# Performance work log

Hardware: AMD Instinct MI355X
Metric: run time of the kernel (lower is better)

Reference implementation:

```python
import jax, jax.numpy as jnp
import numpy as np

B, P, E = 256, 196, 2048           # batch, num_pixels, encoder_size
H, A, EMB = 2048, 512, 300         # hidden, attention, embedding dims
V_IN, V_OUT = 262, 261             # input vocab (classes+2), output (classes+1)
T = 7                              # max_seq_len + 2


def setup_inputs() -> dict:
    key = jax.random.key(0)
    ks = jax.random.split(key, 20)
    s = 0.02
    return {
        "encoder_feature_out": jax.random.normal(ks[0], (B, P, E), jnp.float32),
        "encoder_out": jax.random.normal(ks[1], (B, E), jnp.float32),
        "annotations_X": jax.random.randint(ks[2], (B, T), 0, V_IN),
        "is_train": 1,
        "emb_W": jax.random.normal(ks[3], (V_IN, EMB), jnp.float32) * s,
        "feat_W": jax.random.normal(ks[4], (H, E), jnp.float32) * s,
        "feat_b": jnp.zeros((H,), jnp.float32),
        "W_ih": jax.random.normal(ks[5], (4 * H, EMB + E), jnp.float32) * s,
        "W_hh": jax.random.normal(ks[6], (4 * H, H), jnp.float32) * s,
        "b_ih": jnp.zeros((4 * H,), jnp.float32),
        "b_hh": jnp.zeros((4 * H,), jnp.float32),
        "enc_att_W": jax.random.normal(ks[7], (A, E), jnp.float32) * s,
        "enc_att_b": jnp.zeros((A,), jnp.float32),
        "dec_att_W": jax.random.normal(ks[8], (A, H), jnp.float32) * s,
        "dec_att_b": jnp.zeros((A,), jnp.float32),
        "full_att_W": jax.random.normal(ks[9], (1, A), jnp.float32) * s,
        "full_att_b": jnp.zeros((1,), jnp.float32),
        "fbeta_W": jax.random.normal(ks[10], (E, H), jnp.float32) * s,
        "fbeta_b": jnp.zeros((E,), jnp.float32),
        "fc_W": jax.random.normal(ks[11], (V_OUT, H), jnp.float32) * s,
        "fc_b": jnp.zeros((V_OUT,), jnp.float32),
    }


def _forward(encoder_feature_out, encoder_out, annotations_X,
             emb_W, feat_W, feat_b, W_ih, W_hh, b_ih, b_hh,
             enc_att_W, enc_att_b, dec_att_W, dec_att_b,
             full_att_W, full_att_b, fbeta_W, fbeta_b, fc_W, fc_b):
    enc = encoder_feature_out                                  # (B,P,E)
    # encoder side of additive attention is constant across steps
    att1 = jnp.einsum('bpe,ae->bpa', enc, enc_att_W) + enc_att_b  # (B,P,A)
    h0 = encoder_out @ feat_W.T + feat_b                       # (B,H)
    c0 = jnp.zeros_like(h0)

    def step(carry, ann_t):
        h, c = carry
        # additive attention
        att2 = h @ dec_att_W.T + dec_att_b                     # (B,A)
        e = jax.nn.relu(att1 + att2[:, None, :]) @ full_att_W[0] + full_att_b[0]  # (B,P)
        alpha = jax.nn.softmax(e, axis=1)                      # (B,P)
        awe = jnp.einsum('bp,bpe->be', alpha, enc)             # (B,E)
        gate = jax.nn.sigmoid(h @ fbeta_W.T + fbeta_b)         # (B,E)
        awe = gate * awe
        # LSTMCell (dropout layers in eval mode -> identity)
        x = jnp.concatenate([emb_W[ann_t], awe], axis=1)       # (B,EMB+E)
        gates = x @ W_ih.T + b_ih + h @ W_hh.T + b_hh          # (B,4H)
        i, f, g, o = jnp.split(gates, 4, axis=1)
        c = jax.nn.sigmoid(f) * c + jax.nn.sigmoid(i) * jnp.tanh(g)
        h = jax.nn.sigmoid(o) * jnp.tanh(c)
        yhat = h @ fc_W.T + fc_b                               # (B,V_OUT)
        return (h, c), (yhat, alpha)

    _, (yhats, alphas) = jax.lax.scan(step, (h0, c0), annotations_X.T)  # (T,B,...)
    return jnp.transpose(yhats, (1, 0, 2)), jnp.transpose(alphas, (1, 0, 2))


def reference(encoder_feature_out, encoder_out, annotations_X, is_train,
              emb_W, feat_W, feat_b, W_ih, W_hh, b_ih, b_hh,
              enc_att_W, enc_att_b, dec_att_W, dec_att_b,
              full_att_W, full_att_b, fbeta_W, fbeta_b, fc_W, fc_b):
    # is_train=True (teacher forcing) path
    return _forward(encoder_feature_out, encoder_out, annotations_X,
                    emb_W, feat_W, feat_b, W_ih, W_hh, b_ih, b_hh,
                    enc_att_W, enc_att_b, dec_att_W, dec_att_b,
                    full_att_W, full_att_b, fbeta_W, fbeta_b, fc_W, fc_b)
```

## Files before the change

### kernel.cpp

```cpp
#include <hip/hip_runtime.h>
#include <math.h>

#define B_    256
#define P_    196
#define E_    2048
#define H_    2048
#define A_    512
#define EMB_  300
#define VOUT_ 261
#define T_    7

#define KPAD_   4608
#define EMBOFF_ 2048
#define AWEOFF_ 2352

#define NSTEP_  2880
#define FCOFF_  2560
#define GSPLIT_ 4
#define PSPLIT_ 2

typedef __attribute__((ext_vector_type(8))) short          short8_t;
typedef __attribute__((ext_vector_type(8))) unsigned short ushort8_t;
typedef __attribute__((ext_vector_type(4))) float          f32x4;

__device__ __forceinline__ unsigned short f2b(float f) {
    union { float f; unsigned int u; } v; v.f = f;
    unsigned int x = v.u;
    unsigned int r = (x + 0x7fffu + ((x >> 16) & 1u)) >> 16;
    return (unsigned short)r;
}
__device__ __forceinline__ float b2f(unsigned short u) {
    union { unsigned int u; float f; } v; v.u = ((unsigned int)u) << 16;
    return v.f;
}
__device__ __forceinline__ ushort8_t pack8(float4 u0, float4 u1) {
    ushort8_t u;
    u[0]=f2b(u0.x); u[1]=f2b(u0.y); u[2]=f2b(u0.z); u[3]=f2b(u0.w);
    u[4]=f2b(u1.x); u[5]=f2b(u1.y); u[6]=f2b(u1.z); u[7]=f2b(u1.w);
    return u;
}

template<bool SPLITK, bool OUT16, bool XCDSWZ>
__global__ __launch_bounds__(256)
void gemm_sk(const unsigned short* __restrict__ Ab, int lda,
             const unsigned short* __restrict__ Bw, int ldb,
             void* __restrict__ Cout, int ldc,
             int Kper, int colbase, const float* __restrict__ bias, int nbx)
{
    __shared__ ushort8_t As8[256 * 8];
    __shared__ ushort8_t Bs8[64 * 8];

    const int tid  = threadIdx.x;
    const int lane = tid & 63;
    const int w    = tid >> 6;

    int nblk, mblk;
    if (XCDSWZ) {
        const int bid  = blockIdx.x;
        const int pair = (bid & 7) * (gridDim.x >> 3) + (bid >> 3);
        nblk = pair % nbx;
        mblk = pair / nbx;
    } else {
        nblk = blockIdx.x;
        mblk = 0;
    }
    const int col0  = colbase + nblk * 64;
    const int kbase = SPLITK ? blockIdx.y * Kper : 0;
    const int mrow0 = XCDSWZ ? mblk * 256 : 0;

    const int rb  = tid >> 3;
    const int seg = tid & 7;
    const int swz = seg ^ (rb & 7);

    const unsigned short* Ap = Ab + (size_t)(mrow0 + rb) * lda + kbase + seg * 8;
    const unsigned short* Bp = Bw + (size_t)(col0 + rb) * ldb + kbase + seg * 8;

    const int lr = lane & 15;
    const int hi = lane >> 4;

    f32x4 acc[4][4];
    #pragma unroll
    for (int m = 0; m < 4; ++m)
        #pragma unroll
        for (int n = 0; n < 4; ++n)
            acc[m][n] = (f32x4){0.f, 0.f, 0.f, 0.f};

    ushort8_t aR[8], bR[2];
    #pragma unroll
    for (int i = 0; i < 8; ++i)
        aR[i] = *(const ushort8_t*)(Ap + (size_t)i * 32 * lda);
    bR[0] = *(const ushort8_t*)(Bp);
    bR[1] = *(const ushort8_t*)(Bp + (size_t)32 * ldb);

    for (int k0 = 0; k0 < Kper; k0 += 64) {
        __syncthreads();
        #pragma unroll
        for (int i = 0; i < 8; ++i)
            As8[(rb + i * 32) * 8 + swz] = aR[i];
        Bs8[rb * 8 + swz]        = bR[0];
        Bs8[(rb + 32) * 8 + swz] = bR[1];
        __syncthreads();
        if (k0 + 64 < Kper) {
            #pragma unroll
            for (int i = 0; i < 8; ++i)
                aR[i] = *(const ushort8_t*)(Ap + (size_t)i * 32 * lda + k0 + 64);
            bR[0] = *(const ushort8_t*)(Bp + k0 + 64);
            bR[1] = *(const ushort8_t*)(Bp + (size_t)32 * ldb + k0 + 64);
        }
        #pragma unroll
        for (int kc = 0; kc < 2; ++kc) {
            short8_t af[4], bf[4];
            #pragma unroll
            for (int m = 0; m < 4; ++m) {
                const int row = w * 64 + m * 16 + lr;
                af[m] = *(const short8_t*)&As8[row * 8 + ((kc * 4 + hi) ^ (row & 7))];
            }
            #pragma unroll
            for (int n = 0; n < 4; ++n) {
                const int row = n * 16 + lr;
                bf[n] = *(const short8_t*)&Bs8[row * 8 + ((kc * 4 + hi) ^ (row & 7))];
            }
            #pragma unroll
            for (int m = 0; m < 4; ++m)
                #pragma unroll
                for (int n = 0; n < 4; ++n)
                    acc[m][n] = __builtin_amdgcn_mfma_f32_16x16x32_bf16(
                        af[m], bf[n], acc[m][n], 0, 0, 0);
        }
    }

    if (OUT16) {
        unsigned short* C16 = (unsigned short*)Cout;
        #pragma unroll
        for (int m = 0; m < 4; ++m) {
            const int grow0 = mrow0 + w * 64 + m * 16 + hi * 4;
            #pragma unroll
            for (int n = 0; n < 4; ++n) {
                const int gcol = col0 + n * 16 + lr;
                const float bv = bias[gcol];
                #pragma unroll
                for (int r = 0; r < 4; ++r)
                    C16[(size_t)(grow0 + r) * ldc + gcol] = f2b(acc[m][n][r] + bv);
            }
        }
    } else {
        float* Cs = (float*)Cout + (SPLITK ? (size_t)blockIdx.y * 256 * ldc : 0);
        #pragma unroll
        for (int m = 0; m < 4; ++m) {
            const int grow0 = w * 64 + m * 16 + hi * 4;
            #pragma unroll
            for (int n = 0; n < 4; ++n) {
                const int gcol = col0 + n * 16 + lr;
                #pragma unroll
                for (int r = 0; r < 4; ++r)
                    Cs[(size_t)(grow0 + r) * ldc + gcol] = acc[m][n][r];
            }
        }
    }
}

__global__ __launch_bounds__(256)
void gemm_mfma_f32(const float* __restrict__ Af, int lda,
                   const unsigned short* __restrict__ Bw, int ldb,
                   unsigned short* __restrict__ Cp, int ldc,
                   const float* __restrict__ bias,
                   int M, int N, int K)
{
    __shared__ __align__(16) unsigned short As[64][40];
    __shared__ __align__(16) unsigned short Bs[128][40];

    const int tid  = threadIdx.x;
    const int lane = tid & 63;
    const int wid  = tid >> 6;
    const int wr   = wid >> 1;
    const int wc   = wid & 1;
    const int row0 = blockIdx.y * 64;
    const int col0 = blockIdx.x * 128;

    const int ar = tid >> 2;
    const int as = (tid & 3) * 8;
    const int br = tid >> 1;
    const int bs = (tid & 1) * 16;

    const int lr = lane & 15;
    const int lk = (lane >> 4) * 8;

    f32x4 acc[2][4];
    #pragma unroll
    for (int m = 0; m < 2; ++m)
        #pragma unroll
        for (int n = 0; n < 4; ++n)
            acc[m][n] = (f32x4){0.f, 0.f, 0.f, 0.f};

    for (int k0 = 0; k0 < K; k0 += 32) {
        ushort8_t aval = {0,0,0,0,0,0,0,0};
        if (row0 + ar < M) {
            const float* p = Af + (size_t)(row0 + ar) * lda + k0 + as;
            aval = pack8(*(const float4*)(p), *(const float4*)(p + 4));
        }
        ushort8_t bv0 = {0,0,0,0,0,0,0,0}, bv1 = {0,0,0,0,0,0,0,0};
        if (col0 + br < N) {
            const unsigned short* p = Bw + (size_t)(col0 + br) * ldb + k0 + bs;
            bv0 = *(const ushort8_t*)(p);
            bv1 = *(const ushort8_t*)(p + 8);
        }
        __syncthreads();
        *(ushort8_t*)&As[ar][as]     = aval;
        *(ushort8_t*)&Bs[br][bs]     = bv0;
        *(ushort8_t*)&Bs[br][bs + 8] = bv1;
        __syncthreads();

        short8_t af[2], bf[4];
        #pragma unroll
        for (int m = 0; m < 2; ++m)
            af[m] = *(const short8_t*)&As[wr * 32 + m * 16 + lr][lk];
        #pragma unroll
        for (int n = 0; n < 4; ++n)
            bf[n] = *(const short8_t*)&Bs[wc * 64 + n * 16 + lr][lk];
        #pragma unroll
        for (int m = 0; m < 2; ++m)
            #pragma unroll
            for (int n = 0; n < 4; ++n)
                acc[m][n] = __builtin_amdgcn_mfma_f32_16x16x32_bf16(
                    af[m], bf[n], acc[m][n], 0, 0, 0);
    }

    #pragma unroll
    for (int m = 0; m < 2; ++m) {
        const int grow0 = row0 + wr * 32 + m * 16 + (lane >> 4) * 4;
        #pragma unroll
        for (int n = 0; n < 4; ++n) {
            const int gcol = col0 + wc * 64 + n * 16 + lr;
            if (gcol >= N) continue;
            const float bv = bias[gcol];
            #pragma unroll
            for (int r = 0; r < 4; ++r) {
                const int grow = grow0 + r;
                if (grow >= M) continue;
                Cp[(size_t)grow * ldc + gcol] = f2b(acc[m][n][r] + bv);
            }
        }
    }
}

__global__ __launch_bounds__(256)
void cvt_bf16_kernel(const float* __restrict__ in, unsigned short* __restrict__ out,
                     int n8)
{
    const int idx = blockIdx.x * 256 + threadIdx.x;
    if (idx >= n8) return;
    const size_t base = (size_t)idx * 8;
    *(ushort8_t*)(out + base) =
        pack8(*(const float4*)(in + base), *(const float4*)(in + base + 4));
}

__global__ __launch_bounds__(256)
void setup_kernel(const float* __restrict__ b_ih, const float* __restrict__ b_hh,
                  float* __restrict__ bias4h,
                  const float* __restrict__ enc_attW, unsigned short* __restrict__ encattW16,
                  const float* __restrict__ feat_W, unsigned short* __restrict__ featW16,
                  const float* __restrict__ enc_out, unsigned short* __restrict__ encout16,
                  const float* __restrict__ dec_attW, const float* __restrict__ fbeta_W,
                  const float* __restrict__ fc_W, unsigned short* __restrict__ wstep,
                  unsigned short* __restrict__ xcat, float* __restrict__ cbuf)
{
    int bid = blockIdx.x;
    const int tid = threadIdx.x;
    if (bid < 32) {
        const int i = bid * 256 + tid;
        bias4h[i] = b_ih[i] + b_hh[i];
        return;
    }
    bid -= 32;
    if (bid < 512) {
        const size_t base = ((size_t)bid * 256 + tid) * 8;
        *(ushort8_t*)(encattW16 + base) =
            pack8(*(const float4*)(enc_attW + base), *(const float4*)(enc_attW + base + 4));
        return;
    }
    bid -= 512;
    if (bid < 2048) {
        const size_t base = ((size_t)bid * 256 + tid) * 8;
        *(ushort8_t*)(featW16 + base) =
            pack8(*(const float4*)(feat_W + base), *(const float4*)(feat_W + base + 4));
        return;
    }
    bid -= 2048;
    if (bid < 256) {
        const size_t base = ((size_t)bid * 256 + tid) * 8;
        *(ushort8_t*)(encout16 + base) =
            pack8(*(const float4*)(enc_out + base), *(const float4*)(enc_out + base + 4));
        return;
    }
    bid -= 256;
    if (bid < NSTEP_) {
        const int row = bid;
        const int c0  = tid * 8;
        const float* src;
        if (row < A_)                   src = dec_attW + (size_t)row * H_ + c0;
        else if (row < A_ + E_)         src = fbeta_W + (size_t)(row - A_) * H_ + c0;
        else if (row < A_ + E_ + VOUT_) src = fc_W + (size_t)(row - A_ - E_) * H_ + c0;
        else                            src = nullptr;
        ushort8_t u = {0,0,0,0,0,0,0,0};
        if (src) u = pack8(*(const float4*)(src), *(const float4*)(src + 4));
        *(ushort8_t*)(wstep + (size_t)row * H_ + c0) = u;
        return;
    }
    bid -= NSTEP_;
    if (bid < 576) {
        const size_t base = ((size_t)bid * 256 + tid) * 8;
        ushort8_t z = {0,0,0,0,0,0,0,0};
        *(ushort8_t*)(xcat + base) = z;
        return;
    }
    bid -= 576;
    {
        const size_t base = ((size_t)bid * 256 + tid) * 4;
        *(float4*)(cbuf + base) = make_float4(0.f, 0.f, 0.f, 0.f);
    }
}

__global__ __launch_bounds__(256)
void build_wcat_kernel(const float* __restrict__ W_ih, const float* __restrict__ W_hh,
                       unsigned short* __restrict__ wcat)
{
    const int row = blockIdx.x;
    const int LIH = EMB_ + E_;
    for (int s = threadIdx.x; s < KPAD_ / 8; s += 256) {
        const int k0 = s * 8;
        ushort8_t u;
        const float* src = nullptr;
        if (k0 + 8 <= H_)                         src = W_hh + (size_t)row * H_ + k0;
        else if (k0 >= H_ && k0 + 8 <= 2344)      src = W_ih + (size_t)row * LIH + (k0 - H_);
        else if (k0 >= AWEOFF_ && k0 + 8 <= 4400) src = W_ih + (size_t)row * LIH + (k0 - 2052);
        if (src) {
            u = pack8(*(const float4*)(src), *(const float4*)(src + 4));
        } else {
            #pragma unroll
            for (int i = 0; i < 8; ++i) {
                const int k = k0 + i;
                float v = 0.f;
                if (k >= H_ && k < 2348)           v = W_ih[(size_t)row * LIH + (k - H_)];
                else if (k >= AWEOFF_ && k < 4400) v = W_ih[(size_t)row * LIH + (k - 2052)];
                u[i] = f2b(v);
            }
        }
        *(ushort8_t*)(wcat + (size_t)row * KPAD_ + k0) = u;
    }
}

__global__ __launch_bounds__(256)
void reduce_h0(const float* __restrict__ parts, const float* __restrict__ bias,
               unsigned short* __restrict__ xcat)
{
    const int i = blockIdx.x * 256 + threadIdx.x;
    const int row = i >> 11, col = i & (H_ - 1);
    float acc = bias[col];
    #pragma unroll
    for (int s = 0; s < 8; ++s)
        acc += parts[(size_t)s * 256 * H_ + i];
    xcat[(size_t)row * KPAD_ + col] = f2b(acc);
}

__global__ __launch_bounds__(256)
void att_awe_kernel(const float* __restrict__ parts, const float* __restrict__ dec_attb,
                    const unsigned short* __restrict__ att1,
                    const float* __restrict__ fw_g, const float* __restrict__ fb,
                    const float* __restrict__ encf, const unsigned short* __restrict__ enc16,
                    int use16,
                    float* __restrict__ awe_part, float* __restrict__ out_a, int t)
{
    const int ph = blockIdx.x;
    const int b  = blockIdx.y;
    const int tid = threadIdx.x;
    const int lane = tid & 63;
    const int wid  = tid >> 6;
    __shared__ float att2s[A_];
    __shared__ float es[P_];
    __shared__ float red[4];

    #pragma unroll
    for (int it = 0; it < A_ / 256; ++it) {
        const int c = tid + it * 256;
        float acc = dec_attb[c];
        #pragma unroll
        for (int s = 0; s < 8; ++s)
            acc += parts[((size_t)s * B_ + b) * NSTEP_ + c];
        att2s[c] = acc;
    }
    __syncthreads();

    const int l32  = lane & 31;
    const int slot = wid * 2 + (lane >> 5);
    float a2r[16], fwr[16];
    #pragma unroll
    for (int k = 0; k < 16; ++k) {
        a2r[k] = att2s[l32 * 16 + k];
        fwr[k] = fw_g[l32 * 16 + k];
    }
    const float fbv = fb[0];

    for (int p = slot; p < P_; p += 8) {
        const unsigned short* row = att1 + ((size_t)b * P_ + p) * A_ + l32 * 16;
        ushort8_t v0 = *(const ushort8_t*)(row);
        ushort8_t v1 = *(const ushort8_t*)(row + 8);
        float acc = 0.f;
        #pragma unroll
        for (int k = 0; k < 8; ++k) {
            float x = b2f(v0[k]) + a2r[k];
            x = x > 0.f ? x : 0.f;
            acc = fmaf(x, fwr[k], acc);
        }
        #pragma unroll
        for (int k = 0; k < 8; ++k) {
            float x = b2f(v1[k]) + a2r[k + 8];
            x = x > 0.f ? x : 0.f;
            acc = fmaf(x, fwr[k + 8], acc);
        }
        #pragma unroll
        for (int off = 16; off > 0; off >>= 1)
            acc += __shfl_xor(acc, off);
        if (l32 == 0) es[p] = acc + fbv;
    }
    __syncthreads();

    float v = (tid < P_) ? es[tid] : -1e30f;
    float m = v;
    #pragma unroll
    for (int off = 32; off > 0; off >>= 1)
        m = fmaxf(m, __shfl_xor(m, off));
    if (lane == 0) red[wid] = m;
    __syncthreads();
    m = fmaxf(fmaxf(red[0], red[1]), fmaxf(red[2], red[3]));
    __syncthreads();
    float p = (tid < P_) ? expf(v - m) : 0.f;
    float s = p;
    #pragma unroll
    for (int off = 32; off > 0; off >>= 1)
        s += __shfl_xor(s, off);
    if (lane == 0) red[wid] = s;
    __syncthreads();
    s = red[0] + red[1] + red[2] + red[3];
    float alv = p / s;
    if (tid < P_) {
        if (ph == 0)
            out_a[((size_t)b * T_ + t) * P_ + tid] = alv;
    }
    __syncthreads();
    if (tid < P_) es[tid] = alv;
    __syncthreads();

    const int e0 = tid * 8;
    const int prow0 = ph * 98;
    float acc[8] = {0.f,0.f,0.f,0.f,0.f,0.f,0.f,0.f};
    if (use16) {
        const unsigned short* ep = enc16 + ((size_t)b * P_ + prow0) * E_ + e0;
        int pp = 0;
        for (; pp + 4 <= 98; pp += 4) {
            ushort8_t v0 = *(const ushort8_t*)(ep + (size_t)(pp + 0) * E_);
            ushort8_t v1 = *(const ushort8_t*)(ep + (size_t)(pp + 1) * E_);
            ushort8_t v2 = *(const ushort8_t*)(ep + (size_t)(pp + 2) * E_);
            ushort8_t v3 = *(const ushort8_t*)(ep + (size_t)(pp + 3) * E_);
            const float a0 = es[prow0 + pp],     a1 = es[prow0 + pp + 1];
            const float a2 = es[prow0 + pp + 2], a3 = es[prow0 + pp + 3];
            #pragma unroll
            for (int k = 0; k < 8; ++k) {
                float t0 = fmaf(a0, b2f(v0[k]), acc[k]);
                float t1 = fmaf(a1, b2f(v1[k]), t0);
                float t2 = fmaf(a2, b2f(v2[k]), t1);
                acc[k]   = fmaf(a3, b2f(v3[k]), t2);
            }
        }
        for (; pp < 98; ++pp) {
            ushort8_t v0 = *(const ushort8_t*)(ep + (size_t)pp * E_);
            const float a0 = es[prow0 + pp];
            #pragma unroll
            for (int k = 0; k < 8; ++k)
                acc[k] = fmaf(a0, b2f(v0[k]), acc[k]);
        }
    } else {
        const float* ep = encf + ((size_t)b * P_ + prow0) * E_ + e0;
        for (int pp = 0; pp < 98; ++pp) {
            float4 v0 = *(const float4*)(ep + (size_t)pp * E_);
            float4 v1 = *(const float4*)(ep + (size_t)pp * E_ + 4);
            const float a0 = es[prow0 + pp];
            acc[0] = fmaf(a0, v0.x, acc[0]); acc[1] = fmaf(a0, v0.y, acc[1]);
            acc[2] = fmaf(a0, v0.z, acc[2]); acc[3] = fmaf(a0, v0.w, acc[3]);
            acc[4] = fmaf(a0, v1.x, acc[4]); acc[5] = fmaf(a0, v1.y, acc[5]);
            acc[6] = fmaf(a0, v1.z, acc[6]); acc[7] = fmaf(a0, v1.w, acc[7]);
        }
    }
    float* dst = awe_part + ((size_t)ph * B_ + b) * E_ + e0;
    *(float4*)(dst)     = make_float4(acc[0], acc[1], acc[2], acc[3]);
    *(float4*)(dst + 4) = make_float4(acc[4], acc[5], acc[6], acc[7]);
}

__global__ __launch_bounds__(256)
void awe_fin_kernel(const float* __restrict__ parts, const float* __restrict__ fbeta_b,
                    const float* __restrict__ awe_part,
                    const int* __restrict__ ann, const float* __restrict__ embW,
                    unsigned short* __restrict__ xcat,
                    const float* __restrict__ fc_b, float* __restrict__ out_y, int t)
{
    const int b = blockIdx.x;
    const int tid = threadIdx.x;
    const int e0 = tid * 8;

    float aw[8] = {0.f,0.f,0.f,0.f,0.f,0.f,0.f,0.f};
    #pragma unroll
    for (int ph = 0; ph < PSPLIT_; ++ph) {
        float4 pa = *(const float4*)(awe_part + ((size_t)ph * B_ + b) * E_ + e0);
        float4 pb = *(const float4*)(awe_part + ((size_t)ph * B_ + b) * E_ + e0 + 4);
        aw[0] += pa.x; aw[1] += pa.y; aw[2] += pa.z; aw[3] += pa.w;
        aw[4] += pb.x; aw[5] += pb.y; aw[6] += pb.z; aw[7] += pb.w;
    }

    ushort8_t o;
    #pragma unroll
    for (int k = 0; k < 8; ++k) {
        float g = fbeta_b[e0 + k];
        #pragma unroll
        for (int s = 0; s < 8; ++s)
            g += parts[((size_t)s * B_ + b) * NSTEP_ + A_ + e0 + k];
        const float sg = 1.f / (1.f + expf(-g));
        o[k] = f2b(sg * aw[k]);
    }
    *(ushort8_t*)(xcat + (size_t)b * KPAD_ + AWEOFF_ + e0) = o;

    const int r = ann[b * T_ + t];
    for (int j = tid; j < EMB_; j += 256)
        xcat[(size_t)b * KPAD_ + EMBOFF_ + j] = f2b(embW[(size_t)r * EMB_ + j]);

    if (t > 0) {
        for (int c = tid; c < VOUT_; c += 256) {
            float a = fc_b[c];
            #pragma unroll
            for (int s = 0; s < 8; ++s)
                a += parts[((size_t)s * B_ + b) * NSTEP_ + FCOFF_ + c];
            out_y[((size_t)b * T_ + (t - 1)) * VOUT_ + c] = a;
        }
    }
}

__global__ __launch_bounds__(256)
void fc_reduce(const float* __restrict__ parts, const float* __restrict__ fc_b,
               float* __restrict__ out_y, int tm1)
{
    const int i = blockIdx.x * 256 + threadIdx.x;
    if (i >= B_ * VOUT_) return;
    const int b = i / VOUT_;
    const int c = i - b * VOUT_;
    float acc = fc_b[c];
    #pragma unroll
    for (int s = 0; s < 8; ++s)
        acc += parts[((size_t)s * B_ + b) * NSTEP_ + FCOFF_ + c];
    out_y[((size_t)b * T_ + tm1) * VOUT_ + c] = acc;
}

__global__ __launch_bounds__(256)
void lstm_kernel(const float* __restrict__ parts, const float* __restrict__ bias4h,
                 float* __restrict__ c, unsigned short* __restrict__ xcat)
{
    const int idx = blockIdx.x * 256 + threadIdx.x;
    const int b = idx >> 11;
    const int j = idx & (H_ - 1);
    const float* p0 = parts + (size_t)b * 4 * H_;
    const size_t S = (size_t)256 * 4 * H_;
    float gi = bias4h[j],          gf = bias4h[H_ + j];
    float gg = bias4h[2 * H_ + j], go = bias4h[3 * H_ + j];
    #pragma unroll
    for (int s = 0; s < GSPLIT_; ++s) {
        const float* p = p0 + s * S;
        gi += p[j]; gf += p[H_ + j]; gg += p[2 * H_ + j]; go += p[3 * H_ + j];
    }
    const float si = 1.f / (1.f + expf(-gi));
    const float sf = 1.f / (1.f + expf(-gf));
    const float so = 1.f / (1.f + expf(-go));
    const float cn = sf * c[idx] + si * tanhf(gg);
    c[idx] = cn;
    xcat[(size_t)b * KPAD_ + j] = f2b(so * tanhf(cn));
}

extern "C" void kernel_launch(void* const* d_in, const int* in_sizes, int n_in,
                              void* d_out, int out_size, void* d_ws, size_t ws_size,
                              hipStream_t stream)
{
    const float* enc      = (const float*)d_in[0];
    const float* enc_out  = (const float*)d_in[1];
    const int*   ann      = (const int*)  d_in[2];
    const float* emb_W    = (const float*)d_in[4];
    const float* feat_W   = (const float*)d_in[5];
    const float* feat_b   = (const float*)d_in[6];
    const float* W_ih     = (const float*)d_in[7];
    const float* W_hh     = (const float*)d_in[8];
    const float* b_ih     = (const float*)d_in[9];
    const float* b_hh     = (const float*)d_in[10];
    const float* enc_attW = (const float*)d_in[11];
    const float* enc_attb = (const float*)d_in[12];
    const float* dec_attW = (const float*)d_in[13];
    const float* dec_attb = (const float*)d_in[14];
    const float* full_attW= (const float*)d_in[15];
    const float* full_attb= (const float*)d_in[16];
    const float* fbeta_W  = (const float*)d_in[17];
    const float* fbeta_b  = (const float*)d_in[18];
    const float* fc_W     = (const float*)d_in[19];
    const float* fc_b     = (const float*)d_in[20];
    (void)in_sizes; (void)n_in; (void)out_size;

    float* out   = (float*)d_out;
    float* out_y = out;
    float* out_a = out + (size_t)B_ * T_ * VOUT_;

    char* base = (char*)d_ws;
    size_t off = 0;
    auto alloc = [&](size_t bytes) -> char* {
        char* p = base + off;
        off += (bytes + 255) & ~(size_t)255;
        return p;
    };
    unsigned short* att1_16   = (unsigned short*)alloc((size_t)B_ * P_ * A_ * 2);
    unsigned short* wcat16    = (unsigned short*)alloc((size_t)4 * H_ * KPAD_ * 2);
    unsigned short* wstep16   = (unsigned short*)alloc((size_t)NSTEP_ * H_ * 2);
    unsigned short* encattW16 = (unsigned short*)alloc((size_t)A_ * E_ * 2);
    unsigned short* featW16   = (unsigned short*)alloc((size_t)H_ * E_ * 2);
    unsigned short* encout16  = (unsigned short*)alloc((size_t)B_ * E_ * 2);
    unsigned short* xcat16    = (unsigned short*)alloc((size_t)B_ * KPAD_ * 2);
    float* cbuf     = (float*)alloc((size_t)B_ * H_ * 4);
    float* bias4h   = (float*)alloc((size_t)4 * H_ * 4);
    float* awe_part = (float*)alloc((size_t)PSPLIT_ * B_ * E_ * 4);
    const size_t parts_elems = (size_t)GSPLIT_ * B_ * 4 * H_;
    float* parts   = (float*)alloc(parts_elems * 4);
    const size_t enc_elems = (size_t)B_ * P_ * E_;
    const int use16 = (off + enc_elems * 2 <= ws_size) ? 1 : 0;
    unsigned short* enc16 = use16 ? (unsigned short*)alloc(enc_elems * 2) : nullptr;

    const dim3 blk(256);

    setup_kernel<<<dim3(32 + 512 + 2048 + 256 + NSTEP_ + 576 + 512), blk, 0, stream>>>(
        b_ih, b_hh, bias4h, enc_attW, encattW16, feat_W, featW16,
        enc_out, encout16, dec_attW, fbeta_W, fc_W, wstep16, xcat16, cbuf);
    build_wcat_kernel<<<dim3(4 * H_), blk, 0, stream>>>(W_ih, W_hh, wcat16);
    if (use16)
        cvt_bf16_kernel<<<dim3((int)(enc_elems / 8 + 255) / 256), blk, 0, stream>>>(
            enc, enc16, (int)(enc_elems / 8));

    if (use16) {
        gemm_sk<false, true, true><<<dim3(196 * 8), blk, 0, stream>>>(
            enc16, E_, encattW16, E_, att1_16, A_, E_, 0, enc_attb, 8);
    } else {
        dim3 g((A_ + 127) / 128, (B_ * P_) / 64);
        gemm_mfma_f32<<<g, blk, 0, stream>>>(enc, E_, encattW16, E_,
            att1_16, A_, enc_attb, B_ * P_, A_, E_);
    }
    gemm_sk<true, false, false><<<dim3(H_ / 64, 8), blk, 0, stream>>>(
        encout16, E_, featW16, E_, parts, H_, E_ / 8, 0, nullptr, 0);
    reduce_h0<<<dim3(B_ * H_ / 256), blk, 0, stream>>>(parts, feat_b, xcat16);

    for (int t = 0; t <= T_; ++t) {
        if (t < T_)
            gemm_sk<true, false, false><<<dim3(NSTEP_ / 64, 8), blk, 0, stream>>>(
                xcat16, KPAD_, wstep16, H_, parts, NSTEP_, H_ / 8, 0, nullptr, 0);
        else
            gemm_sk<true, false, false><<<dim3((NSTEP_ - FCOFF_) / 64, 8), blk, 0, stream>>>(
                xcat16, KPAD_, wstep16, H_, parts, NSTEP_, H_ / 8, FCOFF_, nullptr, 0);
        if (t == T_) {
            fc_reduce<<<dim3((B_ * VOUT_ + 255) / 256), blk, 0, stream>>>(parts, fc_b, out_y, t - 1);
            break;
        }

        att_awe_kernel<<<dim3(PSPLIT_, B_), blk, 0, stream>>>(
            parts, dec_attb, att1_16, full_attW, full_attb,
            enc, enc16, use16, awe_part, out_a, t);
        awe_fin_kernel<<<dim3(B_), blk, 0, stream>>>(parts, fbeta_b, awe_part,
                                                     ann, emb_W, xcat16, fc_b, out_y, t);

        gemm_sk<true, false, false><<<dim3(4 * H_ / 64, GSPLIT_), blk, 0, stream>>>(
            xcat16, KPAD_, wcat16, KPAD_, parts, 4 * H_, KPAD_ / GSPLIT_, 0, nullptr, 0);
        lstm_kernel<<<dim3(B_ * H_ / 256), blk, 0, stream>>>(parts, bias4h, cbuf, xcat16);
    }
}
```

Baseline: 1.197 ms.

## Double-buffer GEMM tiles with direct global-to-LDS async loads

The bf16 MFMA GEMM now loads its A and B tiles straight from global memory into shared memory with `global_load_lds`, instead of staging them through registers. It ping-pongs two LDS buffers so the next K-slice is fetched while the current one is computed. The XOR swizzle moves from the LDS store address to the global source column, so the LDS read pattern is unchanged. This removes register pressure and the VGPR-to-LDS store instructions, at the cost of double the LDS footprint. The loop assumes an even number of K steps and relies on the barriers correctly waiting for the async loads.

```diff
diff --git a/kernel.cpp b/kernel.cpp
--- a/kernel.cpp
+++ b/kernel.cpp
@@ -40,6 +40,13 @@
     return u;
 }
 
+__device__ __forceinline__ void gld_lds16(const unsigned short* g, const ushort8_t* l) {
+    __builtin_amdgcn_global_load_lds(
+        (const __attribute__((address_space(1))) void*)g,
+        (__attribute__((address_space(3))) void*)l,
+        16, 0, 0);
+}
+
 template<bool SPLITK, bool OUT16, bool XCDSWZ>
 __global__ __launch_bounds__(256)
 void gemm_sk(const unsigned short* __restrict__ Ab, int lda,
@@ -47,8 +54,8 @@
              void* __restrict__ Cout, int ldc,
              int Kper, int colbase, const float* __restrict__ bias, int nbx)
 {
-    __shared__ ushort8_t As8[256 * 8];
-    __shared__ ushort8_t Bs8[64 * 8];
+    __shared__ ushort8_t As8[2][256 * 8];
+    __shared__ ushort8_t Bs8[2][64 * 8];
 
     const int tid  = threadIdx.x;
     const int lane = tid & 63;
@@ -72,8 +79,8 @@
     const int seg = tid & 7;
     const int swz = seg ^ (rb & 7);
 
-    const unsigned short* Ap = Ab + (size_t)(mrow0 + rb) * lda + kbase + seg * 8;
-    const unsigned short* Bp = Bw + (size_t)(col0 + rb) * ldb + kbase + seg * 8;
+    const unsigned short* Ap = Ab + (size_t)(mrow0 + rb) * lda + kbase + swz * 8;
+    const unsigned short* Bp = Bw + (size_t)(col0 + rb) * ldb + kbase + swz * 8;
 
     const int lr = lane & 15;
     const int hi = lane >> 4;
@@ -85,40 +92,29 @@
         for (int n = 0; n < 4; ++n)
             acc[m][n] = (f32x4){0.f, 0.f, 0.f, 0.f};
 
-    ushort8_t aR[8], bR[2];
-    #pragma unroll
-    for (int i = 0; i < 8; ++i)
-        aR[i] = *(const ushort8_t*)(Ap + (size_t)i * 32 * lda);
-    bR[0] = *(const ushort8_t*)(Bp);
-    bR[1] = *(const ushort8_t*)(Bp + (size_t)32 * ldb);
-
-    for (int k0 = 0; k0 < Kper; k0 += 64) {
-        __syncthreads();
+    auto STAGE = [&](int buf, int koff) {
         #pragma unroll
         for (int i = 0; i < 8; ++i)
-            As8[(rb + i * 32) * 8 + swz] = aR[i];
-        Bs8[rb * 8 + swz]        = bR[0];
-        Bs8[(rb + 32) * 8 + swz] = bR[1];
-        __syncthreads();
-        if (k0 + 64 < Kper) {
-            #pragma unroll
-            for (int i = 0; i < 8; ++i)
-                aR[i] = *(const ushort8_t*)(Ap + (size_t)i * 32 * lda + k0 + 64);
-            bR[0] = *(const ushort8_t*)(Bp + k0 + 64);
-            bR[1] = *(const ushort8_t*)(Bp + (size_t)32 * ldb + k0 + 64);
-        }
+            gld_lds16(Ap + (size_t)i * 32 * lda + koff,
+                      &As8[buf][(i * 32 + w * 8) * 8]);
+        #pragma unroll
+        for (int j = 0; j < 2; ++j)
+            gld_lds16(Bp + (size_t)j * 32 * ldb + koff,
+                      &Bs8[buf][(j * 32 + w * 8) * 8]);
+    };
+    auto COMPUTE = [&](int buf) {
         #pragma unroll
         for (int kc = 0; kc < 2; ++kc) {
             short8_t af[4], bf[4];
             #pragma unroll
             for (int m = 0; m < 4; ++m) {
                 const int row = w * 64 + m * 16 + lr;
-                af[m] = *(const short8_t*)&As8[row * 8 + ((kc * 4 + hi) ^ (row & 7))];
+                af[m] = *(const short8_t*)&As8[buf][row * 8 + ((kc * 4 + hi) ^ (row & 7))];
             }
             #pragma unroll
             for (int n = 0; n < 4; ++n) {
                 const int row = n * 16 + lr;
-                bf[n] = *(const short8_t*)&Bs8[row * 8 + ((kc * 4 + hi) ^ (row & 7))];
+                bf[n] = *(const short8_t*)&Bs8[buf][row * 8 + ((kc * 4 + hi) ^ (row & 7))];
             }
             #pragma unroll
             for (int m = 0; m < 4; ++m)
@@ -127,6 +123,19 @@
                     acc[m][n] = __builtin_amdgcn_mfma_f32_16x16x32_bf16(
                         af[m], bf[n], acc[m][n], 0, 0, 0);
         }
+    };
+
+    const int nsteps = Kper >> 6;
+    STAGE(0, 0);
+    __syncthreads();
+    for (int s = 0; s < nsteps; s += 2) {
+        STAGE(1, (s + 1) * 64);
+        COMPUTE(0);
+        __syncthreads();
+        if (s + 2 < nsteps)
+            STAGE(0, (s + 2) * 64);
+        COMPUTE(1);
+        __syncthreads();
     }
 
     if (OUT16) {
```

After: 1.314 ms. 9.7% more time.
